# Kernel tuning notes

Hardware: AMD Instinct MI355X
Metric: run time of the kernel (lower is better)

The kernel has to match this reference:

```python
import jax, jax.numpy as jnp
import numpy as np

N, H, E, K, C, M = 4096, 512, 512, 64, 128, 4  # tokens, hidden, embed, categories, children/cat, max_num_children
IN = E + H  # LSTMCell input size


def setup_inputs() -> dict:
    key = jax.random.key(0)
    ks = jax.random.split(key, 12)
    s = 0.05
    return {
        "et": jax.random.normal(ks[0], (N, H), jnp.float32),
        "x": jax.random.normal(ks[1], (N, IN), jnp.float32),
        "h": jax.random.normal(ks[2], (N, H), jnp.float32),
        "c": jax.random.normal(ks[3], (N, H), jnp.float32),
        "cat": jax.random.randint(ks[4], (N,), 0, K, jnp.int32),
        "ci": jax.random.randint(ks[5], (N,), 0, M, jnp.int32),
        # per-category prediction Linear(hidden_size -> |children(category)|)
        "W_lin": jax.random.normal(ks[6], (K, C, H), jnp.float32) * s,
        "b_lin": jax.random.normal(ks[7], (K, C), jnp.float32) * s,
        # per-child-index LSTMCell(embedding+hidden -> hidden), torch gate order i,f,g,o
        "W_ih": jax.random.normal(ks[8], (M, 4 * H, IN), jnp.float32) * s,
        "W_hh": jax.random.normal(ks[9], (M, 4 * H, H), jnp.float32) * s,
        "b_ih": jax.random.normal(ks[10], (M, 4 * H), jnp.float32) * s,
        "b_hh": jax.random.normal(ks[11], (M, 4 * H), jnp.float32) * s,
    }


def reference(et, x, h, c, cat, ci, W_lin, b_lin, W_ih, W_hh, b_ih, b_hh):
    # get_log_odds: route each token to its category's Linear (gather weights, per-token matvec)
    Wg = W_lin[cat]                                   # [N, C, H]
    log_odds = jnp.einsum('nh,nch->nc', et, Wg) + b_lin[cat]  # [N, C]

    # get_next: LSTMCell selected by child_index. Only M=4 cells, so compute all
    # cells' gates densely (efficient GEMMs) and select with a one-hot mix.
    gates_all = (jnp.einsum('ni,kgi->nkg', x, W_ih)
                 + jnp.einsum('nh,kgh->nkg', h, W_hh)
                 + (b_ih + b_hh)[None])               # [N, M, 4H]
    sel = jax.nn.one_hot(ci, M, dtype=gates_all.dtype)  # [N, M]
    gates = jnp.einsum('nkg,nk->ng', gates_all, sel)     # [N, 4H]
    i_, f_, g_, o_ = jnp.split(gates, 4, axis=-1)
    c2 = jax.nn.sigmoid(f_) * c + jax.nn.sigmoid(i_) * jnp.tanh(g_)
    h2 = jax.nn.sigmoid(o_) * jnp.tanh(c2)
    return log_odds, h2, c2
```

## Files before the change

### kernel.cpp

```cpp
#include <hip/hip_runtime.h>
#include <hip/hip_bf16.h>
#include <stdint.h>

#define NTOK 4096
#define HID  512
#define INSZ 1024
#define KIN  1536
#define KCAT 64
#define CCH  128
#define MCELL 4
#define G4H  2048
#define SLOTS 4992

typedef unsigned short u16;
typedef __bf16 bf16x8 __attribute__((ext_vector_type(8)));
typedef float  f32x4  __attribute__((ext_vector_type(4)));

__device__ __forceinline__ u16 f2bf(float f) {
    unsigned u = __float_as_uint(f);
    u += 0x7fffu + ((u >> 16) & 1u);
    return (u16)(u >> 16);
}
__device__ __forceinline__ float bf2f(u16 v) {
    return __uint_as_float(((unsigned)v) << 16);
}
__device__ __forceinline__ void store_bf8(u16* p, float4 a, float4 b) {
    ushort4 r0, r1;
    r0.x = f2bf(a.x); r0.y = f2bf(a.y); r0.z = f2bf(a.z); r0.w = f2bf(a.w);
    r1.x = f2bf(b.x); r1.y = f2bf(b.y); r1.z = f2bf(b.z); r1.w = f2bf(b.w);
    *reinterpret_cast<ushort4*>(p) = r0;
    *reinterpret_cast<ushort4*>(p + 4) = r1;
}
__device__ __forceinline__ void gl16(const u16* g, u16* l) {
    __builtin_amdgcn_global_load_lds((const __attribute__((address_space(1))) void*)g,
                                     (__attribute__((address_space(3))) void*)l, 16, 0, 0);
}

#define CH_W  (8192 * 192)
#define CH_A  (4097 * 192)
#define CH_TOT (CH_W + CH_A)
#define PK_BLOCKS 2048

__global__ __launch_bounds__(256) void fat_pack(
    const float* __restrict__ x, const float* __restrict__ h,
    const float* __restrict__ Wih, const float* __restrict__ Whh,
    const int* __restrict__ ci, const int* __restrict__ cat,
    int* __restrict__ meta, int* __restrict__ perm_ci, int* __restrict__ perm_cat,
    u16* __restrict__ A_tok, u16* __restrict__ Wb)
{
    if (blockIdx.x == 0) {
        __shared__ int cnt_ci[MCELL], cur_ci[MCELL];
        __shared__ int cnt_cat[KCAT], cur_cat[KCAT];
        __shared__ int scan_cat[KCAT];
        int tid = threadIdx.x;
        if (tid < MCELL) cnt_ci[tid] = 0;
        if (tid < KCAT)  cnt_cat[tid] = 0;
        __syncthreads();
        for (int t = tid; t < NTOK; t += 256) {
            atomicAdd(&cnt_ci[ci[t]], 1);
            atomicAdd(&cnt_cat[cat[t]], 1);
        }
        __syncthreads();
        for (int i = tid; i < 128; i += 256) meta[136 + i] = -1;
        if (tid < MCELL) {
            int off = 0;
            for (int i = 0; i < tid; ++i) off += (cnt_ci[i] + 191) / 192 * 192;
            int p = (cnt_ci[tid] + 191) / 192 * 192;
            meta[tid] = p; meta[4 + tid] = off; cur_ci[tid] = off;
        }
        if (tid < KCAT) scan_cat[tid] = (cnt_cat[tid] + 63) & ~63;
        __syncthreads();
        for (int d = 1; d < KCAT; d <<= 1) {
            int v = 0;
            if (tid < KCAT && tid >= d) v = scan_cat[tid - d];
            __syncthreads();
            if (tid < KCAT) scan_cat[tid] += v;
            __syncthreads();
        }
        if (tid < KCAT) {
            int p = (cnt_cat[tid] + 63) & ~63;
            int off = scan_cat[tid] - p;
            meta[8 + tid] = p; meta[72 + tid] = off; cur_cat[tid] = off;
            for (int i = 0; i < p / 64; ++i) meta[136 + off / 64 + i] = tid;
        }
        __syncthreads();
        for (int i = tid; i < SLOTS; i += 256) perm_ci[i] = -1;
        for (int i = tid; i < 8192; i += 256) perm_cat[i] = -1;
        __syncthreads();
        for (int t = tid; t < NTOK; t += 256) {
            perm_ci[atomicAdd(&cur_ci[ci[t]], 1)] = t;
            perm_cat[atomicAdd(&cur_cat[cat[t]], 1)] = t;
        }
        return;
    }
    for (int i = (blockIdx.x - 1) * 256 + threadIdx.x; i < CH_TOT; i += (PK_BLOCKS - 1) * 256) {
        if (i < CH_W) {
            int row = i / 192, cc = i - row * 192;
            int m = row >> 11, j = row & 2047;
            int srow = (j & 3) * HID + (j >> 2);
            int c = cc * 8;
            const float* src = (c < INSZ) ? (Wih + ((size_t)m * G4H + srow) * INSZ + c)
                                          : (Whh + ((size_t)m * G4H + srow) * HID + (c - INSZ));
            store_bf8(Wb + (size_t)row * KIN + c,
                      *(const float4*)src, *(const float4*)(src + 4));
        } else {
            int i3 = i - CH_W;
            int row = i3 / 192, cc = i3 - row * 192;
            int c = cc * 8;
            u16* dst = A_tok + (size_t)row * KIN + c;
            if (row == NTOK) {
                *reinterpret_cast<int4*>(dst) = make_int4(0, 0, 0, 0);
            } else {
                const float* src = (c < INSZ) ? (x + (size_t)row * INSZ + c)
                                              : (h + (size_t)row * HID + (c - INSZ));
                store_bf8(dst, *(const float4*)src, *(const float4*)(src + 4));
            }
        }
    }
}

__global__ __launch_bounds__(512, 2) void mega_gemm(
    const u16* __restrict__ A_tok,
    const u16* __restrict__ Wb,
    const float* __restrict__ W_lin,
    const float* __restrict__ et,
    const float* __restrict__ b_lin,
    const float* __restrict__ c,
    const float* __restrict__ b_ih,
    const float* __restrict__ b_hh,
    const int* __restrict__ meta,
    const int* __restrict__ perm_ci,
    const int* __restrict__ perm_cat,
    float* __restrict__ out)
{
    __shared__ __align__(16) u16 S[28672];
    __shared__ int sperm[192];

    int tid = threadIdx.x;
    int lane = tid & 63;
    int qd = lane >> 4, l15 = lane & 15;
    int rsw = l15 & 7;

    int id = blockIdx.x;
    if (id < 704) {
        int g = id & 31, rt = id >> 5;
        int m = g >> 3, ct = g & 7;
        int pcnt = meta[m];
        if (rt * 192 >= pcnt) return;
        int row0 = meta[4 + m] + rt * 192;

        if (tid < 192) sperm[tid] = perm_ci[row0 + tid];
        __syncthreads();

        const u16* gA[3]; u16* lA[3];
        #pragma unroll
        for (int j = 0; j < 3; ++j) {
            int q = j * 512 + tid;
            int row = q >> 3, kc = (q & 7) ^ (row & 7);
            int t = sperm[row];
            gA[j] = A_tok + (size_t)(t >= 0 ? t : NTOK) * KIN + kc * 8;
            lA[j] = &S[q * 8];
        }
        const u16* gB[4]; u16* lB[4];
        #pragma unroll
        for (int j = 0; j < 4; ++j) {
            int q = j * 512 + tid;
            int row = q >> 3, kc = (q & 7) ^ (row & 7);
            gB[j] = Wb + ((size_t)m * G4H + ct * 256 + row) * KIN + kc * 8;
            lB[j] = &S[12288 + q * 8];
        }

        int wave = tid >> 6;
        int wm = wave >> 2, wn = wave & 3;

        f32x4 acc[6][4];
        #pragma unroll
        for (int i = 0; i < 6; ++i)
            #pragma unroll
            for (int j = 0; j < 4; ++j)
                acc[i][j] = (f32x4){0.f, 0.f, 0.f, 0.f};

        for (int ks = 0; ks < KIN / 64; ++ks) {
            #pragma unroll
            for (int j = 0; j < 3; ++j) { gl16(gA[j], lA[j]); gA[j] += 64; }
            #pragma unroll
            for (int j = 0; j < 4; ++j) { gl16(gB[j], lB[j]); gB[j] += 64; }
            __syncthreads();
            #pragma unroll
            for (int ks2 = 0; ks2 < 2; ++ks2) {
                int ch = (ks2 * 4 + qd) ^ rsw;
                bf16x8 fb[4];
                #pragma unroll
                for (int tj = 0; tj < 4; ++tj) {
                    int row = wn * 64 + tj * 16 + l15;
                    fb[tj] = *reinterpret_cast<const bf16x8*>(&S[12288 + row * 64 + ch * 8]);
                }
                #pragma unroll
                for (int ti = 0; ti < 6; ++ti) {
                    int row = wm * 96 + ti * 16 + l15;
                    bf16x8 fa = *reinterpret_cast<const bf16x8*>(&S[row * 64 + ch * 8]);
                    #pragma unroll
                    for (int tj = 0; tj < 4; ++tj)
                        acc[ti][tj] = __builtin_amdgcn_mfma_f32_16x16x32_bf16(fa, fb[tj], acc[ti][tj], 0, 0, 0);
                }
            }
            __syncthreads();
        }

        int gt = l15 & 3;
        float bias[4];
        #pragma unroll
        for (int tj = 0; tj < 4; ++tj) {
            int u = ct * 64 + wn * 16 + tj * 4 + (l15 >> 2);
            bias[tj] = b_ih[m * G4H + gt * HID + u] + b_hh[m * G4H + gt * HID + u];
        }
        int b0 = lane & 1, b1 = lane & 2;
        const size_t o_h2 = (size_t)NTOK * CCH;
        const size_t o_c2 = o_h2 + (size_t)NTOK * HID;
        #pragma unroll
        for (int ti = 0; ti < 6; ++ti) {
            int t = sperm[wm * 96 + ti * 16 + qd * 4 + (lane & 3)];
            #pragma unroll
            for (int tj = 0; tj < 4; ++tj) {
                float v0 = acc[ti][tj][0] + bias[tj];
                float v1 = acc[ti][tj][1] + bias[tj];
                float v2 = acc[ti][tj][2] + bias[tj];
                float v3 = acc[ti][tj][3] + bias[tj];
                float tmp;
                tmp = __shfl_xor(b0 ? v0 : v1, 1); if (b0) v0 = tmp; else v1 = tmp;
                tmp = __shfl_xor(b0 ? v2 : v3, 1); if (b0) v2 = tmp; else v3 = tmp;
                tmp = __shfl_xor(b1 ? v0 : v2, 2); if (b1) v0 = tmp; else v2 = tmp;
                tmp = __shfl_xor(b1 ? v1 : v3, 2); if (b1) v1 = tmp; else v3 = tmp;
                if (t >= 0) {
                    int u = ct * 64 + wn * 16 + tj * 4 + (l15 >> 2);
                    float si = 1.f / (1.f + __expf(-v0));
                    float sf = 1.f / (1.f + __expf(-v1));
                    float tg = tanhf(v2);
                    float so = 1.f / (1.f + __expf(-v3));
                    float cold = c[(size_t)t * HID + u];
                    float c2 = sf * cold + si * tg;
                    float h2 = so * tanhf(c2);
                    out[o_h2 + (size_t)t * HID + u] = h2;
                    out[o_c2 + (size_t)t * HID + u] = c2;
                }
            }
        }
    } else {
        int half = tid >> 8;
        int tid2 = tid & 255;
        int wave2 = tid2 >> 6;
        u16* As = S + half * 12288;
        u16* Bs = As + 8192;
        int* sp = sperm + half * 64;

        int rtl = (id - 704) * 2 + half;
        int k = meta[136 + rtl];
        int valid = (k >= 0);
        if (!valid) k = 0;
        int r0 = rtl * 64;

        if (tid2 < 64) sp[tid2] = valid ? perm_cat[r0 + tid2] : -1;
        __syncthreads();

        int rb = tid2 >> 3;
        int wkc = (tid2 & 7) ^ (rb & 7);

        const float* wsrc[4]; u16* wdst[4];
        #pragma unroll
        for (int i = 0; i < 4; ++i) {
            wsrc[i] = W_lin + ((size_t)k * CCH + i * 32 + rb) * HID + wkc * 8;
            wdst[i] = As + ((size_t)i * 256 + tid2) * 8;
        }
        int ar = tid2 >> 2;
        int acp = tid2 & 3;
        int at = sp[ar];
        const float* asrc = (at >= 0) ? (et + (size_t)at * HID) : nullptr;

        f32x4 acc[4][2];
        #pragma unroll
        for (int i = 0; i < 4; ++i) {
            acc[i][0] = (f32x4){0.f, 0.f, 0.f, 0.f};
            acc[i][1] = (f32x4){0.f, 0.f, 0.f, 0.f};
        }

        for (int kk = 0; kk < HID; kk += 64) {
            #pragma unroll
            for (int i = 0; i < 4; ++i) {
                const float* s = wsrc[i] + kk;
                store_bf8(wdst[i], *(const float4*)s, *(const float4*)(s + 4));
            }
            #pragma unroll
            for (int j = 0; j < 2; ++j) {
                int dch = acp * 2 + j;
                int sch = dch ^ (ar & 7);
                u16* dst = &Bs[ar * 64 + dch * 8];
                if (asrc) {
                    const float* s = asrc + kk + sch * 8;
                    store_bf8(dst, *(const float4*)s, *(const float4*)(s + 4));
                } else {
                    *reinterpret_cast<int4*>(dst) = make_int4(0, 0, 0, 0);
                }
            }
            __syncthreads();
            #pragma unroll
            for (int ks2 = 0; ks2 < 2; ++ks2) {
                int ch = (ks2 * 4 + qd) ^ rsw;
                bf16x8 fa[4], fb[2];
                #pragma unroll
                for (int ti = 0; ti < 4; ++ti)
                    fa[ti] = *reinterpret_cast<const bf16x8*>(&Bs[(ti * 16 + l15) * 64 + ch * 8]);
                #pragma unroll
                for (int tj = 0; tj < 2; ++tj)
                    fb[tj] = *reinterpret_cast<const bf16x8*>(&As[(wave2 * 32 + tj * 16 + l15) * 64 + ch * 8]);
                #pragma unroll
                for (int ti = 0; ti < 4; ++ti)
                    #pragma unroll
                    for (int tj = 0; tj < 2; ++tj)
                        acc[ti][tj] = __builtin_amdgcn_mfma_f32_16x16x32_bf16(fa[ti], fb[tj], acc[ti][tj], 0, 0, 0);
            }
            __syncthreads();
        }

        #pragma unroll
        for (int ti = 0; ti < 4; ++ti) {
            #pragma unroll
            for (int tj = 0; tj < 2; ++tj) {
                int n = wave2 * 32 + tj * 16 + l15;
                float bias = b_lin[k * CCH + n];
                #pragma unroll
                for (int rr = 0; rr < 4; ++rr) {
                    int row = ti * 16 + qd * 4 + rr;
                    int t = sp[row];
                    if (t >= 0)
                        out[(size_t)t * CCH + n] = acc[ti][tj][rr] + bias;
                }
            }
        }
    }
}

extern "C" void kernel_launch(void* const* d_in, const int* in_sizes, int n_in,
                              void* d_out, int out_size, void* d_ws, size_t ws_size,
                              hipStream_t stream) {
    const float* et    = (const float*)d_in[0];
    const float* x     = (const float*)d_in[1];
    const float* h     = (const float*)d_in[2];
    const float* c     = (const float*)d_in[3];
    const int*   cat   = (const int*)d_in[4];
    const int*   ci    = (const int*)d_in[5];
    const float* W_lin = (const float*)d_in[6];
    const float* b_lin = (const float*)d_in[7];
    const float* W_ih  = (const float*)d_in[8];
    const float* W_hh  = (const float*)d_in[9];
    const float* b_ih  = (const float*)d_in[10];
    const float* b_hh  = (const float*)d_in[11];
    float* out = (float*)d_out;

    char* ws = (char*)d_ws;
    int* meta     = (int*)ws;
    int* perm_ci  = (int*)(ws + 2048);
    int* perm_cat = (int*)(ws + 22528);
    u16* A_tok    = (u16*)(ws + 55296);
    u16* Wb       = (u16*)(ws + 12641280);

    fat_pack<<<PK_BLOCKS, 256, 0, stream>>>(x, h, W_ih, W_hh, ci, cat,
                                            meta, perm_ci, perm_cat, A_tok, Wb);

    mega_gemm<<<704 + 64, 512, 0, stream>>>(A_tok, Wb, W_lin, et, b_lin, c,
                                            b_ih, b_hh, meta, perm_ci, perm_cat, out);
}
```

Baseline: 221.5 us.

## Double-buffer LSTM GEMM in LDS with 256-row tiles and phased MFMA scheduling

```diff
diff --git a/kernel.cpp b/kernel.cpp
--- a/kernel.cpp
+++ b/kernel.cpp
@@ -10,7 +10,7 @@
 #define CCH  128
 #define MCELL 4
 #define G4H  2048
-#define SLOTS 4992
+#define SLOTS 5120
 
 typedef unsigned short u16;
 typedef __bf16 bf16x8 __attribute__((ext_vector_type(8)));
@@ -64,8 +64,8 @@
         for (int i = tid; i < 128; i += 256) meta[136 + i] = -1;
         if (tid < MCELL) {
             int off = 0;
-            for (int i = 0; i < tid; ++i) off += (cnt_ci[i] + 191) / 192 * 192;
-            int p = (cnt_ci[tid] + 191) / 192 * 192;
+            for (int i = 0; i < tid; ++i) off += (cnt_ci[i] + 255) & ~255;
+            int p = (cnt_ci[tid] + 255) & ~255;
             meta[tid] = p; meta[4 + tid] = off; cur_ci[tid] = off;
         }
         if (tid < KCAT) scan_cat[tid] = (cnt_cat[tid] + 63) & ~63;
@@ -119,6 +119,8 @@
     }
 }
 
+#define FENCE() __builtin_amdgcn_sched_barrier(0)
+
 __global__ __launch_bounds__(512, 2) void mega_gemm(
     const u16* __restrict__ A_tok,
     const u16* __restrict__ Wb,
@@ -133,8 +135,8 @@
     const int* __restrict__ perm_cat,
     float* __restrict__ out)
 {
-    __shared__ __align__(16) u16 S[28672];
-    __shared__ int sperm[192];
+    __shared__ __align__(16) u16 S[65536];
+    __shared__ int sperm[256];
 
     int tid = threadIdx.x;
     int lane = tid & 63;
@@ -142,70 +144,92 @@
     int rsw = l15 & 7;
 
     int id = blockIdx.x;
-    if (id < 704) {
-        int g = id & 31, rt = id >> 5;
-        int m = g >> 3, ct = g & 7;
+    if (id < 256) {
+        int ct = id & 7;
+        int m = (id >> 3) & 3;
+        int rt = id >> 5;
         int pcnt = meta[m];
-        if (rt * 192 >= pcnt) return;
-        int row0 = meta[4 + m] + rt * 192;
-
-        if (tid < 192) sperm[tid] = perm_ci[row0 + tid];
-        __syncthreads();
-
-        const u16* gA[3]; u16* lA[3];
-        #pragma unroll
-        for (int j = 0; j < 3; ++j) {
-            int q = j * 512 + tid;
-            int row = q >> 3, kc = (q & 7) ^ (row & 7);
-            int t = sperm[row];
-            gA[j] = A_tok + (size_t)(t >= 0 ? t : NTOK) * KIN + kc * 8;
-            lA[j] = &S[q * 8];
-        }
-        const u16* gB[4]; u16* lB[4];
+        if (rt * 256 >= pcnt) return;
+        int row0 = meta[4 + m] + rt * 256;
+
+        if (tid < 256) sperm[tid] = perm_ci[row0 + tid];
+        __syncthreads();
+
+        const u16* gA[4]; const u16* gB[4]; int qq[4];
         #pragma unroll
         for (int j = 0; j < 4; ++j) {
             int q = j * 512 + tid;
             int row = q >> 3, kc = (q & 7) ^ (row & 7);
+            int t0 = sperm[row];
+            gA[j] = A_tok + (size_t)(t0 >= 0 ? t0 : NTOK) * KIN + kc * 8;
             gB[j] = Wb + ((size_t)m * G4H + ct * 256 + row) * KIN + kc * 8;
-            lB[j] = &S[12288 + q * 8];
+            qq[j] = q * 8;
         }
 
         int wave = tid >> 6;
         int wm = wave >> 2, wn = wave & 3;
 
-        f32x4 acc[6][4];
-        #pragma unroll
-        for (int i = 0; i < 6; ++i)
+        f32x4 acc[8][4];
+        #pragma unroll
+        for (int i = 0; i < 8; ++i)
             #pragma unroll
             for (int j = 0; j < 4; ++j)
                 acc[i][j] = (f32x4){0.f, 0.f, 0.f, 0.f};
 
-        for (int ks = 0; ks < KIN / 64; ++ks) {
-            #pragma unroll
-            for (int j = 0; j < 3; ++j) { gl16(gA[j], lA[j]); gA[j] += 64; }
-            #pragma unroll
-            for (int j = 0; j < 4; ++j) { gl16(gB[j], lB[j]); gB[j] += 64; }
-            __syncthreads();
-            #pragma unroll
-            for (int ks2 = 0; ks2 < 2; ++ks2) {
-                int ch = (ks2 * 4 + qd) ^ rsw;
-                bf16x8 fb[4];
-                #pragma unroll
-                for (int tj = 0; tj < 4; ++tj) {
-                    int row = wn * 64 + tj * 16 + l15;
-                    fb[tj] = *reinterpret_cast<const bf16x8*>(&S[12288 + row * 64 + ch * 8]);
-                }
-                #pragma unroll
-                for (int ti = 0; ti < 6; ++ti) {
-                    int row = wm * 96 + ti * 16 + l15;
-                    bf16x8 fa = *reinterpret_cast<const bf16x8*>(&S[row * 64 + ch * 8]);
-                    #pragma unroll
-                    for (int tj = 0; tj < 4; ++tj)
-                        acc[ti][tj] = __builtin_amdgcn_mfma_f32_16x16x32_bf16(fa, fb[tj], acc[ti][tj], 0, 0, 0);
-                }
-            }
-            __syncthreads();
-        }
+#define STAGE(NAB) do { \
+        _Pragma("unroll") \
+        for (int j = 0; j < 4; ++j) { gl16(gA[j], &S[(NAB) + qq[j]]); gA[j] += 64; } \
+        _Pragma("unroll") \
+        for (int j = 0; j < 4; ++j) { gl16(gB[j], &S[(NAB) + 16384 + qq[j]]); gB[j] += 64; } \
+    } while (0)
+
+#define PHASE(ks2, tih, AB, STG, NAB, VMW) do { \
+        bf16x8 fa[4], fb[4]; \
+        int ch = ((ks2) * 4 + qd) ^ rsw; \
+        _Pragma("unroll") \
+        for (int tj = 0; tj < 4; ++tj) \
+            fb[tj] = *reinterpret_cast<const bf16x8*>( \
+                &S[(AB) + 16384 + (wn * 64 + tj * 16 + l15) * 64 + ch * 8]); \
+        _Pragma("unroll") \
+        for (int ii = 0; ii < 4; ++ii) \
+            fa[ii] = *reinterpret_cast<const bf16x8*>( \
+                &S[(AB) + (wm * 128 + (tih) * 64 + ii * 16 + l15) * 64 + ch * 8]); \
+        if (STG) STAGE(NAB); \
+        FENCE(); \
+        __builtin_amdgcn_s_barrier(); \
+        FENCE(); \
+        __builtin_amdgcn_s_setprio(1); \
+        _Pragma("unroll") \
+        for (int ii = 0; ii < 4; ++ii) \
+            _Pragma("unroll") \
+            for (int tj = 0; tj < 4; ++tj) \
+                acc[(tih) * 4 + ii][tj] = __builtin_amdgcn_mfma_f32_16x16x32_bf16( \
+                    fa[ii], fb[tj], acc[(tih) * 4 + ii][tj], 0, 0, 0); \
+        __builtin_amdgcn_s_setprio(0); \
+        FENCE(); \
+        if (VMW) asm volatile("s_waitcnt vmcnt(0)" ::: "memory"); \
+        __builtin_amdgcn_s_barrier(); \
+        FENCE(); \
+    } while (0)
+
+#define KTILE(AB, NAB, STG) do { \
+        PHASE(0, 0, AB, STG, NAB, 0); \
+        PHASE(0, 1, AB, 0,   0,   0); \
+        PHASE(1, 0, AB, 0,   0,   0); \
+        PHASE(1, 1, AB, 0,   0,   1); \
+    } while (0)
+
+        STAGE(0);
+        asm volatile("s_waitcnt vmcnt(0)" ::: "memory");
+        __syncthreads();
+        #pragma unroll 1
+        for (int tt = 0; tt < 12; ++tt) {
+            KTILE(0, 32768, 1);
+            KTILE(32768, 0, (tt < 11));
+        }
+#undef KTILE
+#undef PHASE
+#undef STAGE
 
         int gt = l15 & 3;
         float bias[4];
@@ -218,8 +242,8 @@
         const size_t o_h2 = (size_t)NTOK * CCH;
         const size_t o_c2 = o_h2 + (size_t)NTOK * HID;
         #pragma unroll
-        for (int ti = 0; ti < 6; ++ti) {
-            int t = sperm[wm * 96 + ti * 16 + qd * 4 + (lane & 3)];
+        for (int ti = 0; ti < 8; ++ti) {
+            int t = sperm[wm * 128 + ti * 16 + qd * 4 + (lane & 3)];
             #pragma unroll
             for (int tj = 0; tj < 4; ++tj) {
                 float v0 = acc[ti][tj][0] + bias[tj];
@@ -253,7 +277,7 @@
         u16* Bs = As + 8192;
         int* sp = sperm + half * 64;
 
-        int rtl = (id - 704) * 2 + half;
+        int rtl = (id - 256) * 2 + half;
         int k = meta[136 + rtl];
         int valid = (k >= 0);
         if (!valid) k = 0;
@@ -366,6 +390,6 @@
     fat_pack<<<PK_BLOCKS, 256, 0, stream>>>(x, h, W_ih, W_hh, ci, cat,
                                             meta, perm_ci, perm_cat, A_tok, Wb);
 
-    mega_gemm<<<704 + 64, 512, 0, stream>>>(A_tok, Wb, W_lin, et, b_lin, c,
+    mega_gemm<<<256 + 64, 512, 0, stream>>>(A_tok, Wb, W_lin, et, b_lin, c,
                                             b_ih, b_hh, meta, perm_ci, perm_cat, out);
 }
```

Result: slower. 240.8 us (+8.7%).
